# Kernel optimization log

Measured on AMD Instinct MI355X. Metric: run time of the kernel, lower is better.

Reference implementation:

```python
import jax, jax.numpy as jnp
import numpy as np

T, S, D = 64, 1024, 2048
BETA = 1.0
NORM = float(np.sqrt(D))  # dimension ** 0.5


def setup_inputs() -> dict:
    key = jax.random.key(0)
    k1, k2, k3, k4, k5 = jax.random.split(key, 5)
    return {
        "time": jax.random.uniform(k1, (T,), dtype=jnp.float32),
        "x_0": jax.random.normal(k2, (D, 1), dtype=jnp.float32),
        "nu": jax.random.normal(k3, (D,), dtype=jnp.float32),
        "Psi": jax.random.normal(k4, (D, D), dtype=jnp.float32),
        "eps": jax.random.normal(k5, (S, D), dtype=jnp.float32),
    }


def reference(time, x_0, nu, Psi, eps):
    # Cholesky-like factor: strictly-lower Psi + unit diagonal
    chol = jnp.tril(Psi, -1) + jnp.eye(D, dtype=Psi.dtype)
    # reparameterized sample: exp((eps @ chol + nu) / sqrt(D))  -> [S, D]
    phi = jnp.exp((eps @ chol + nu[None, :]) / NORM)
    # diag(phi @ phi.T) == row-wise squared norms (avoid SxS gram)
    row_sq = jnp.sum(phi * phi, axis=1)  # [S]
    # compute_sigma_s(phi): per-sample decay rate = squared row norm (assumed)
    sigma = row_sq  # [S]
    # decoder
    x0phi = phi @ x_0  # [S, 1]
    weights = x0phi / row_sq[:, None]  # [S, 1]
    fea_vec = phi * weights  # [S, D]
    exp_decay = jnp.exp(-BETA * time[:, None] * sigma[None, :])  # [T, S]
    x_t_pred = exp_decay[:, :, None] * fea_vec[None, :, :]  # [T, S, D]
    # soft constraint: diagonal of x_t_pred @ phi.T over (dim1, dim2)
    diag = jnp.einsum('tsd,sd->ts', x_t_pred, phi)  # [T, S]
    x0xt_pred = (diag * diag) / row_sq[None, :]  # [T, S]
    return (x_t_pred.astype(jnp.float32), x0xt_pred, phi)
```

## Files before the change

### kernel.cpp

```cpp
#include <hip/hip_runtime.h>
#include <hip/hip_bf16.h>

#define T_DIM 64
#define S_DIM 1024
#define D_DIM 2048

#define INV_NORM 0.022097086912079608f

__global__ __launch_bounds__(256) void gemm_phi_kernel(
    const float* __restrict__ eps,
    const float* __restrict__ Psi,
    const float* __restrict__ nu,
    float* __restrict__ phi)
{
    __shared__ float As[16][68];
    __shared__ float Bs[16][68];

    const int bn = blockIdx.x;
    const int bm = blockIdx.y;
    const int tid = threadIdx.x;
    const int tx = tid & 15;
    const int ty = tid >> 4;
    const int row0 = bm * 64;
    const int col0 = bn * 64;

    const int a_row = tid >> 2;
    const int a_k   = (tid & 3) * 4;
    const int b_k = tid >> 4;
    const int b_j = (tid & 15) * 4;

    float c[4][4] = {};

    for (int k0 = col0; k0 < D_DIM; k0 += 16) {
        const float4 av = *(const float4*)&eps[(size_t)(row0 + a_row) * D_DIM + k0 + a_k];

        const int gi = k0 + b_k;
        const int gj = col0 + b_j;
        const float4 bv = *(const float4*)&Psi[(size_t)gi * D_DIM + gj];
        float b0 = (gi > gj    ) ? bv.x : ((gi == gj    ) ? 1.0f : 0.0f);
        float b1 = (gi > gj + 1) ? bv.y : ((gi == gj + 1) ? 1.0f : 0.0f);
        float b2 = (gi > gj + 2) ? bv.z : ((gi == gj + 2) ? 1.0f : 0.0f);
        float b3 = (gi > gj + 3) ? bv.w : ((gi == gj + 3) ? 1.0f : 0.0f);

        __syncthreads();

        As[a_k + 0][a_row] = av.x;
        As[a_k + 1][a_row] = av.y;
        As[a_k + 2][a_row] = av.z;
        As[a_k + 3][a_row] = av.w;
        *(float4*)&Bs[b_k][b_j] = make_float4(b0, b1, b2, b3);

        __syncthreads();

        #pragma unroll
        for (int kk = 0; kk < 16; ++kk) {
            const float4 a4 = *(const float4*)&As[kk][ty * 4];
            const float4 b4 = *(const float4*)&Bs[kk][tx * 4];
            const float ar[4] = {a4.x, a4.y, a4.z, a4.w};
            const float br[4] = {b4.x, b4.y, b4.z, b4.w};
            #pragma unroll
            for (int i = 0; i < 4; ++i)
                #pragma unroll
                for (int j = 0; j < 4; ++j)
                    c[i][j] = fmaf(ar[i], br[j], c[i][j]);
        }
    }

    const float4 nu4 = *(const float4*)&nu[col0 + tx * 4];
    #pragma unroll
    for (int i = 0; i < 4; ++i) {
        const int s = row0 + ty * 4 + i;
        float4 o;
        o.x = expf((c[i][0] + nu4.x) * INV_NORM);
        o.y = expf((c[i][1] + nu4.y) * INV_NORM);
        o.z = expf((c[i][2] + nu4.z) * INV_NORM);
        o.w = expf((c[i][3] + nu4.w) * INV_NORM);
        *(float4*)&phi[(size_t)s * D_DIM + col0 + tx * 4] = o;
    }
}

__global__ __launch_bounds__(256) void row_stats_kernel(
    const float* __restrict__ phi,
    const float* __restrict__ x0,
    float* __restrict__ row_sq,
    float* __restrict__ x0phi)
{
    const int s = blockIdx.x;
    const int tid = threadIdx.x;

    float sq = 0.0f, xp = 0.0f;
    #pragma unroll
    for (int base = 0; base < D_DIM; base += 1024) {
        const int d = base + tid * 4;
        const float4 p = *(const float4*)&phi[(size_t)s * D_DIM + d];
        const float4 x = *(const float4*)&x0[d];
        sq += p.x * p.x + p.y * p.y + p.z * p.z + p.w * p.w;
        xp += p.x * x.x + p.y * x.y + p.z * x.z + p.w * x.w;
    }

    #pragma unroll
    for (int off = 32; off > 0; off >>= 1) {
        sq += __shfl_down(sq, off);
        xp += __shfl_down(xp, off);
    }

    __shared__ float ssq[4];
    __shared__ float sxp[4];
    if ((tid & 63) == 0) {
        ssq[tid >> 6] = sq;
        sxp[tid >> 6] = xp;
    }
    __syncthreads();
    if (tid == 0) {
        row_sq[s] = ssq[0] + ssq[1] + ssq[2] + ssq[3];
        x0phi[s]  = sxp[0] + sxp[1] + sxp[2] + sxp[3];
    }
}

__global__ __launch_bounds__(256) void decode_kernel(
    const float* __restrict__ phi,
    const float* __restrict__ time,
    const float* __restrict__ row_sq,
    const float* __restrict__ x0phi,
    float* __restrict__ x_t,
    float* __restrict__ x0xt)
{
    const int s = blockIdx.x;
    const int tid = threadIdx.x;

    __shared__ float st[T_DIM];
    if (tid < T_DIM) st[tid] = time[tid];

    const float sigma = row_sq[s];
    const float xp = x0phi[s];
    const float w = xp / sigma;

    const float4 p0 = *(const float4*)&phi[(size_t)s * D_DIM + tid * 4];
    const float4 p1 = *(const float4*)&phi[(size_t)s * D_DIM + 1024 + tid * 4];
    float4 f0, f1;
    f0.x = w * p0.x; f0.y = w * p0.y; f0.z = w * p0.z; f0.w = w * p0.w;
    f1.x = w * p1.x; f1.y = w * p1.y; f1.z = w * p1.z; f1.w = w * p1.w;

    __syncthreads();

    #pragma unroll 4
    for (int t = 0; t < T_DIM; ++t) {
        const float e = expf(-st[t] * sigma);
        float4 o0, o1;
        o0.x = e * f0.x; o0.y = e * f0.y; o0.z = e * f0.z; o0.w = e * f0.w;
        o1.x = e * f1.x; o1.y = e * f1.y; o1.z = e * f1.z; o1.w = e * f1.w;
        float* dst = &x_t[((size_t)t * S_DIM + s) * D_DIM];
        *(float4*)&dst[tid * 4] = o0;
        *(float4*)&dst[1024 + tid * 4] = o1;
    }

    if (tid < T_DIM) {
        const float e = expf(-st[tid] * sigma);
        const float diag = e * xp;
        x0xt[(size_t)tid * S_DIM + s] = diag * diag / sigma;
    }
}

extern "C" void kernel_launch(void* const* d_in, const int* in_sizes, int n_in,
                              void* d_out, int out_size, void* d_ws, size_t ws_size,
                              hipStream_t stream) {
    const float* time = (const float*)d_in[0];
    const float* x0   = (const float*)d_in[1];
    const float* nu   = (const float*)d_in[2];
    const float* Psi  = (const float*)d_in[3];
    const float* eps  = (const float*)d_in[4];

    float* out = (float*)d_out;
    float* x_t  = out;
    float* x0xt = out + (size_t)T_DIM * S_DIM * D_DIM;
    float* phi  = x0xt + (size_t)T_DIM * S_DIM;

    float* row_sq = (float*)d_ws;
    float* x0phi  = row_sq + S_DIM;

    dim3 gemm_grid(D_DIM / 64, S_DIM / 64);
    gemm_phi_kernel<<<gemm_grid, 256, 0, stream>>>(eps, Psi, nu, phi);
    row_stats_kernel<<<S_DIM, 256, 0, stream>>>(phi, x0, row_sq, x0phi);
    decode_kernel<<<S_DIM, 256, 0, stream>>>(phi, time, row_sq, x0phi, x_t, x0xt);
}
```

Before: 766.7 us.

## Replace FP32 SIMT GEMM with split-bf16 MFMA GEMM and pre-split operands

Replaces the scalar FP32 tiled GEMM for eps @ chol with an MFMA bf16 GEMM that uses a hi/lo split (three products per tile) to approximate FP32 accuracy. Two new prep kernels split eps into bf16 hi/lo and build the transposed, masked Cholesky factor in bf16 hi/lo. The GEMM uses 128x128 tiles with swizzled LDS and register prefetching, and skips the all-zero k-range below the diagonal. This adds extra kernels and workspace traffic, and the dropped lo*lo term causes a small accuracy loss. The decode stage, which is likely dominated by writing the large output, is unchanged.

Measured after the change: 700.0 us. 1.1x faster.

```diff
diff --git a/kernel.cpp b/kernel.cpp
--- a/kernel.cpp
+++ b/kernel.cpp
@@ -7,75 +7,180 @@
 
 #define INV_NORM 0.022097086912079608f
 
-__global__ __launch_bounds__(256) void gemm_phi_kernel(
+typedef __attribute__((ext_vector_type(8))) short     bf16x8;
+typedef __attribute__((ext_vector_type(4))) float     f32x4;
+typedef __attribute__((ext_vector_type(8))) unsigned short u16x8;
+typedef __attribute__((ext_vector_type(4))) unsigned short u16x4;
+
+static __device__ inline unsigned short f2bf(float x) {
+    __hip_bfloat16 b = __float2bfloat16(x);
+    return *reinterpret_cast<unsigned short*>(&b);
+}
+static __device__ inline float bf2f(unsigned short u) {
+    __hip_bfloat16 b = *reinterpret_cast<__hip_bfloat16*>(&u);
+    return __bfloat162float(b);
+}
+static __device__ inline void split2(float x, unsigned short& h, unsigned short& l) {
+    h = f2bf(x);
+    l = f2bf(x - bf2f(h));
+}
+
+__global__ __launch_bounds__(256) void prep_eps_kernel(
     const float* __restrict__ eps,
+    unsigned short* __restrict__ Ah, unsigned short* __restrict__ Al)
+{
+    const int idx = (blockIdx.x * 256 + threadIdx.x) * 4;
+    const float4 v = *(const float4*)&eps[idx];
+    u16x4 h, l;
+    unsigned short* hp = (unsigned short*)&h;
+    unsigned short* lp = (unsigned short*)&l;
+    split2(v.x, hp[0], lp[0]);
+    split2(v.y, hp[1], lp[1]);
+    split2(v.z, hp[2], lp[2]);
+    split2(v.w, hp[3], lp[3]);
+    *(u16x4*)&Ah[idx] = h;
+    *(u16x4*)&Al[idx] = l;
+}
+
+__global__ __launch_bounds__(256) void prep_chol_kernel(
     const float* __restrict__ Psi,
-    const float* __restrict__ nu,
-    float* __restrict__ phi)
-{
-    __shared__ float As[16][68];
-    __shared__ float Bs[16][68];
-
-    const int bn = blockIdx.x;
-    const int bm = blockIdx.y;
-    const int tid = threadIdx.x;
-    const int tx = tid & 15;
-    const int ty = tid >> 4;
-    const int row0 = bm * 64;
-    const int col0 = bn * 64;
-
-    const int a_row = tid >> 2;
-    const int a_k   = (tid & 3) * 4;
-    const int b_k = tid >> 4;
-    const int b_j = (tid & 15) * 4;
-
-    float c[4][4] = {};
-
-    for (int k0 = col0; k0 < D_DIM; k0 += 16) {
-        const float4 av = *(const float4*)&eps[(size_t)(row0 + a_row) * D_DIM + k0 + a_k];
-
-        const int gi = k0 + b_k;
-        const int gj = col0 + b_j;
-        const float4 bv = *(const float4*)&Psi[(size_t)gi * D_DIM + gj];
-        float b0 = (gi > gj    ) ? bv.x : ((gi == gj    ) ? 1.0f : 0.0f);
-        float b1 = (gi > gj + 1) ? bv.y : ((gi == gj + 1) ? 1.0f : 0.0f);
-        float b2 = (gi > gj + 2) ? bv.z : ((gi == gj + 2) ? 1.0f : 0.0f);
-        float b3 = (gi > gj + 3) ? bv.w : ((gi == gj + 3) ? 1.0f : 0.0f);
-
+    unsigned short* __restrict__ Bh, unsigned short* __restrict__ Bl)
+{
+    __shared__ float tile[64][65];
+    const int k0 = blockIdx.x * 64;
+    const int n0 = blockIdx.y * 64;
+    const int tid = threadIdx.x;
+    const int tr = tid >> 4;
+    const int tc = (tid & 15) * 4;
+
+    #pragma unroll
+    for (int p = 0; p < 4; ++p) {
+        const int r = p * 16 + tr;
+        const float4 v = *(const float4*)&Psi[(size_t)(k0 + r) * D_DIM + n0 + tc];
+        tile[r][tc + 0] = v.x;
+        tile[r][tc + 1] = v.y;
+        tile[r][tc + 2] = v.z;
+        tile[r][tc + 3] = v.w;
+    }
+    __syncthreads();
+
+    #pragma unroll
+    for (int p = 0; p < 4; ++p) {
+        const int nl = p * 16 + tr;
+        const int kl = tc;
+        const int gn = n0 + nl;
+        u16x4 h, l;
+        unsigned short* hp = (unsigned short*)&h;
+        unsigned short* lp = (unsigned short*)&l;
+        #pragma unroll
+        for (int i = 0; i < 4; ++i) {
+            const int gk = k0 + kl + i;
+            float v = tile[kl + i][nl];
+            v = (gk > gn) ? v : ((gk == gn) ? 1.0f : 0.0f);
+            split2(v, hp[i], lp[i]);
+        }
+        *(u16x4*)&Bh[(size_t)gn * D_DIM + k0 + kl] = h;
+        *(u16x4*)&Bl[(size_t)gn * D_DIM + k0 + kl] = l;
+    }
+}
+
+#define BM 128
+#define BN 128
+#define BK 32
+
+__global__ __launch_bounds__(256) void gemm_mfma_kernel(
+    const unsigned short* __restrict__ Ah, const unsigned short* __restrict__ Al,
+    const unsigned short* __restrict__ Bh, const unsigned short* __restrict__ Bl,
+    const float* __restrict__ nu, float* __restrict__ phi)
+{
+    __shared__ __align__(16) unsigned short sAh[BM * BK];
+    __shared__ __align__(16) unsigned short sAl[BM * BK];
+    __shared__ __align__(16) unsigned short sBh[BM * BK];
+    __shared__ __align__(16) unsigned short sBl[BM * BK];
+
+    const int tid = threadIdx.x;
+    const int bn = blockIdx.x, bm = blockIdx.y;
+    const int row0 = bm * BM, col0 = bn * BN;
+    const int lane = tid & 63, w = tid >> 6;
+    const int wr = w >> 1, wc = w & 1;
+
+    const int sr = tid >> 1;
+    const int sh = tid & 1;
+    const size_t gA = (size_t)(row0 + sr) * D_DIM;
+    const size_t gB = (size_t)(col0 + sr) * D_DIM;
+    const int swz = (sr & 3) << 4;
+    const int ldsOff0 = sr * 64 + ((sh * 32 +  0) ^ swz);
+    const int ldsOff1 = sr * 64 + ((sh * 32 + 16) ^ swz);
+    const int eOff0 = sh * 16;
+    const int eOff1 = sh * 16 + 8;
+
+    u16x8 rAh0, rAh1, rAl0, rAl1, rBh0, rBh1, rBl0, rBl1;
+
+#define LOADG(k)  do {                                              \
+        rAh0 = *(const u16x8*)&Ah[gA + (k) + eOff0];                \
+        rAh1 = *(const u16x8*)&Ah[gA + (k) + eOff1];                \
+        rAl0 = *(const u16x8*)&Al[gA + (k) + eOff0];                \
+        rAl1 = *(const u16x8*)&Al[gA + (k) + eOff1];                \
+        rBh0 = *(const u16x8*)&Bh[gB + (k) + eOff0];                \
+        rBh1 = *(const u16x8*)&Bh[gB + (k) + eOff1];                \
+        rBl0 = *(const u16x8*)&Bl[gB + (k) + eOff0];                \
+        rBl1 = *(const u16x8*)&Bl[gB + (k) + eOff1];                \
+    } while (0)
+
+    f32x4 acc[4][4] = {};
+
+    LOADG(col0);
+    for (int k0 = col0; k0 < D_DIM; k0 += BK) {
         __syncthreads();
-
-        As[a_k + 0][a_row] = av.x;
-        As[a_k + 1][a_row] = av.y;
-        As[a_k + 2][a_row] = av.z;
-        As[a_k + 3][a_row] = av.w;
-        *(float4*)&Bs[b_k][b_j] = make_float4(b0, b1, b2, b3);
-
+        *(u16x8*)((char*)sAh + ldsOff0) = rAh0;
+        *(u16x8*)((char*)sAh + ldsOff1) = rAh1;
+        *(u16x8*)((char*)sAl + ldsOff0) = rAl0;
+        *(u16x8*)((char*)sAl + ldsOff1) = rAl1;
+        *(u16x8*)((char*)sBh + ldsOff0) = rBh0;
+        *(u16x8*)((char*)sBh + ldsOff1) = rBh1;
+        *(u16x8*)((char*)sBl + ldsOff0) = rBl0;
+        *(u16x8*)((char*)sBl + ldsOff1) = rBl1;
         __syncthreads();
 
-        #pragma unroll
-        for (int kk = 0; kk < 16; ++kk) {
-            const float4 a4 = *(const float4*)&As[kk][ty * 4];
-            const float4 b4 = *(const float4*)&Bs[kk][tx * 4];
-            const float ar[4] = {a4.x, a4.y, a4.z, a4.w};
-            const float br[4] = {b4.x, b4.y, b4.z, b4.w};
+        if (k0 + BK < D_DIM) LOADG(k0 + BK);
+
+        bf16x8 ah[4], al[4], bh[4], bl[4];
+        const int cb = (lane >> 4) * 16;
+        #pragma unroll
+        for (int f = 0; f < 4; ++f) {
+            const int rA = wr * 64 + f * 16 + (lane & 15);
+            const int aoff = rA * 64 + (cb ^ ((rA & 3) << 4));
+            ah[f] = *(const bf16x8*)((const char*)sAh + aoff);
+            al[f] = *(const bf16x8*)((const char*)sAl + aoff);
+            const int rB = wc * 64 + f * 16 + (lane & 15);
+            const int boff = rB * 64 + (cb ^ ((rB & 3) << 4));
+            bh[f] = *(const bf16x8*)((const char*)sBh + boff);
+            bl[f] = *(const bf16x8*)((const char*)sBl + boff);
+        }
+
+        #pragma unroll
+        for (int i = 0; i < 4; ++i)
             #pragma unroll
-            for (int i = 0; i < 4; ++i)
-                #pragma unroll
-                for (int j = 0; j < 4; ++j)
-                    c[i][j] = fmaf(ar[i], br[j], c[i][j]);
+            for (int j = 0; j < 4; ++j) {
+                acc[i][j] = __builtin_amdgcn_mfma_f32_16x16x32_bf16(ah[i], bh[j], acc[i][j], 0, 0, 0);
+                acc[i][j] = __builtin_amdgcn_mfma_f32_16x16x32_bf16(ah[i], bl[j], acc[i][j], 0, 0, 0);
+                acc[i][j] = __builtin_amdgcn_mfma_f32_16x16x32_bf16(al[i], bh[j], acc[i][j], 0, 0, 0);
+            }
+    }
+#undef LOADG
+
+    #pragma unroll
+    for (int j = 0; j < 4; ++j) {
+        const int col = col0 + wc * 64 + j * 16 + (lane & 15);
+        const float nuv = nu[col];
+        #pragma unroll
+        for (int i = 0; i < 4; ++i) {
+            const int rbase = row0 + wr * 64 + i * 16 + (lane >> 4) * 4;
+            #pragma unroll
+            for (int r = 0; r < 4; ++r)
+                phi[(size_t)(rbase + r) * D_DIM + col] =
+                    expf((acc[i][j][r] + nuv) * INV_NORM);
         }
-    }
-
-    const float4 nu4 = *(const float4*)&nu[col0 + tx * 4];
-    #pragma unroll
-    for (int i = 0; i < 4; ++i) {
-        const int s = row0 + ty * 4 + i;
-        float4 o;
-        o.x = expf((c[i][0] + nu4.x) * INV_NORM);
-        o.y = expf((c[i][1] + nu4.y) * INV_NORM);
-        o.z = expf((c[i][2] + nu4.z) * INV_NORM);
-        o.w = expf((c[i][3] + nu4.w) * INV_NORM);
-        *(float4*)&phi[(size_t)s * D_DIM + col0 + tx * 4] = o;
     }
 }
 
@@ -175,11 +280,16 @@
     float* x0xt = out + (size_t)T_DIM * S_DIM * D_DIM;
     float* phi  = x0xt + (size_t)T_DIM * S_DIM;
 
-    float* row_sq = (float*)d_ws;
+    unsigned short* Ah = (unsigned short*)d_ws;
+    unsigned short* Al = Ah + (size_t)S_DIM * D_DIM;
+    unsigned short* Bh = Al + (size_t)S_DIM * D_DIM;
+    unsigned short* Bl = Bh + (size_t)D_DIM * D_DIM;
+    float* row_sq = (float*)(Bl + (size_t)D_DIM * D_DIM);
     float* x0phi  = row_sq + S_DIM;
 
-    dim3 gemm_grid(D_DIM / 64, S_DIM / 64);
-    gemm_phi_kernel<<<gemm_grid, 256, 0, stream>>>(eps, Psi, nu, phi);
+    prep_eps_kernel<<<(S_DIM * D_DIM) / (256 * 4), 256, 0, stream>>>(eps, Ah, Al);
+    prep_chol_kernel<<<dim3(D_DIM / 64, D_DIM / 64), 256, 0, stream>>>(Psi, Bh, Bl);
+    gemm_mfma_kernel<<<dim3(D_DIM / BN, S_DIM / BM), 256, 0, stream>>>(Ah, Al, Bh, Bl, nu, phi);
     row_stats_kernel<<<S_DIM, 256, 0, stream>>>(phi, x0, row_sq, x0phi);
     decode_kernel<<<S_DIM, 256, 0, stream>>>(phi, time, row_sq, x0phi, x_t, x0xt);
 }
```
